# Kernel tuning notes

Measured on AMD Instinct MI355X. Metric: run time of the kernel, lower is better.

Reference implementation:

```python
import jax, jax.numpy as jnp
import numpy as np


def setup_inputs() -> dict:
    key = jax.random.key(0)
    B, T, FFT, HOP = 16, 2048, 1024, 256
    n_bins = FFT // 2 + 1  # 513
    stfts = jax.random.normal(key, (B, T, n_bins, 2), dtype=jnp.float32)
    return {"stfts": stfts, "frame_length": FFT, "frame_step": HOP, "fft_length": FFT}


def reference(stfts, frame_length, frame_step, fft_length):
    # --- precomputed constants (built in the layer's build()) ---
    n = jnp.arange(fft_length, dtype=jnp.float32)
    angles = (2.0 * np.pi / fft_length) * (n[:, None] * n[None, :])  # [fft, fft]
    idft_cos = jnp.cos(angles)
    idft_sin = jnp.sin(angles)
    # periodic Hann window
    t = jnp.arange(frame_length, dtype=jnp.float32)
    window = 0.5 - 0.5 * jnp.cos(2.0 * np.pi * t / frame_length)
    hop_ratio = frame_step / frame_length
    normalization = np.sqrt(1.0 / (1.0 - hop_ratio + 1e-8))
    syn_window = window / np.float32(normalization)
    if fft_length > frame_length:
        syn_window = jnp.pad(syn_window, (0, fft_length - frame_length))

    # --- forward ---
    real_part = stfts[..., 0]  # [B, T, n_bins]
    imag_part = stfts[..., 1]
    if fft_length % 2 == 0:
        mirror_real = real_part[:, :, 1:-1]
        mirror_imag = imag_part[:, :, 1:-1]
    else:
        mirror_real = real_part[:, :, 1:]
        mirror_imag = imag_part[:, :, 1:]
    full_real = jnp.concatenate([real_part, mirror_real[:, :, ::-1]], axis=-1)   # [B, T, fft]
    full_imag = jnp.concatenate([imag_part, -mirror_imag[:, :, ::-1]], axis=-1)  # [B, T, fft]

    # explicit IDFT via dense matmul (transpose_b in TF; matrices are symmetric)
    time_real = jnp.einsum('btf,nf->btn', full_real, idft_cos)
    time_real = time_real - jnp.einsum('btf,nf->btn', full_imag, idft_sin)
    time_real = time_real / jnp.float32(fft_length)

    windowed = (time_real * syn_window[None, None, :])[:, :, :frame_length]  # [B, T, frame_length]

    # overlap-and-add
    B, T, L = windowed.shape
    out_len = (T - 1) * frame_step + frame_length
    idx = jnp.arange(T)[:, None] * frame_step + jnp.arange(L)[None, :]  # [T, L]
    out = jnp.zeros((B, out_len), dtype=windowed.dtype).at[:, idx].add(windowed)
    return out
```

## Files before the change

### kernel.cpp

```cpp
#include <hip/hip_runtime.h>
#include <math.h>


#define BATCH  16
#define TFR    2048
#define NB     513
#define HOP    256
#define OUTLEN 525056
#define TROWS  2051
#define OWN    32
#define NBLK   65
#define OLALEN (OWN * HOP)
#define OLAPAD (OLALEN + OLALEN / 16)

#define NTHR   512
#define NWAVE  8

#define PIDX(n) ((n) + ((n) >> 4))

#define TWO_PI 6.2831853071795864f
#define WSCALE 8.456302966727588e-4f

__device__ __forceinline__ float2 cadd(float2 a, float2 b){ return make_float2(a.x+b.x, a.y+b.y); }
__device__ __forceinline__ float2 csub(float2 a, float2 b){ return make_float2(a.x-b.x, a.y-b.y); }
__device__ __forceinline__ float2 cmul(float2 a, float2 b){ return make_float2(a.x*b.x - a.y*b.y, a.x*b.y + a.y*b.x); }

#if __has_builtin(__builtin_amdgcn_permlane32_swap)
#define HAVE_PL32 1
__device__ __forceinline__ float plsel32(float v, bool pick0) {
    auto r = __builtin_amdgcn_permlane32_swap(
        __builtin_bit_cast(int, v), __builtin_bit_cast(int, v), false, false);
    return __builtin_bit_cast(float, pick0 ? r[0] : r[1]);
}
#else
#define HAVE_PL32 0
#endif

template<int CTRL>
__device__ __forceinline__ float dppf(float v) {
    return __builtin_bit_cast(float,
        __builtin_amdgcn_update_dpp(0, __builtin_bit_cast(int, v), CTRL, 0xF, 0xF, true));
}

__device__ __forceinline__ float2 bstep(float2 u, float2 p, bool hi, float2 W) {
    const float2 s = cadd(u, p);
    const float2 d = cmul(csub(u, p), W);
    return hi ? d : s;
}

__device__ __constant__ const float W16C[8] = { 1.f, 0.9238795325112867f, 0.7071067811865476f, 0.3826834323650898f,
                                                0.f,-0.3826834323650898f,-0.7071067811865476f,-0.9238795325112867f };
__device__ __constant__ const float W16S[8] = { 0.f, 0.3826834323650898f, 0.7071067811865476f, 0.9238795325112867f,
                                                1.f, 0.9238795325112867f, 0.7071067811865476f, 0.3826834323650898f };
__device__ __constant__ const float CWT[16] = {
    1.f, 0.9999811752826011f, 0.9999247018391445f, 0.9998305817958234f,
    0.9996988186962042f, 0.9995294175010931f, 0.9993223845883495f, 0.9990777277526454f,
    0.9987954562051724f, 0.9984755805732948f, 0.9981181129001492f, 0.9977230666441916f,
    0.9972904566786902f, 0.9968202992911657f, 0.9963126121827780f, 0.9957674144676598f };
__device__ __constant__ const float SWT[16] = {
    0.f, 0.0061358846491545f, 0.0122715382857199f, 0.0184067299058048f,
    0.0245412285229123f, 0.0306748031766366f, 0.0368072229413588f, 0.0429382569349408f,
    0.0490676743274180f, 0.0551952443496899f, 0.0613207363022086f, 0.0674439195636641f,
    0.0735645635996674f, 0.0796824379714301f, 0.0857973123444399f, 0.0919089564971327f };

__global__ __launch_bounds__(NTHR)
void istft_rfft(const float2* __restrict__ stfts, float* __restrict__ out)
{
    __shared__ float ola[OLAPAD];

    const int tid  = threadIdx.x;
    const int lane = tid & 63;
    const int wave = tid >> 6;

    const int b  = blockIdx.x / NBLK;
    const int ib = blockIdx.x - b * NBLK;
    const int T0 = ib * OWN;

    for (int i = tid; i < OLAPAD; i += NTHR) ola[i] = 0.f;

    float2 P, V;
    { float s, c; sincosf(TWO_PI * (float)lane * (1.0f/1024.0f), &s, &c); P = make_float2(c, s); }
    const int brl = ((lane & 1) << 5) | ((lane & 2) << 3) | ((lane & 4) << 1)
                  | ((lane & 8) >> 1) | ((lane & 16) >> 3) | ((lane & 32) >> 5);
    const int n0 = brl * 16;
    { float s, c; sincosf(TWO_PI * (float)n0 * (1.0f/1024.0f), &s, &c); V = make_float2(c, s); }

    const float2 Q   = cmul(P, P);
    const float2 P4  = cmul(Q, Q);
    const float2 P8  = cmul(P4, P4);
    const float2 B64 = cmul(P8, P8);
    const float2 B32 = cmul(B64, B64);
    const float2 B16 = cmul(B32, B32);
    const float2 B8c = cmul(B16, B16);
    const float2 B4c = cmul(B8c, B8c);

#if HAVE_PL32
    bool pick32;
    { auto pr = __builtin_amdgcn_permlane32_swap(lane, lane, false, false);
      pick32 = ((pr[0] == (lane & 31)) == (lane >= 32)); }
#endif
    const bool hi32 = lane >= 32;
    const bool hi16 = (lane & 16) != 0;
    const bool hi8  = (lane & 8)  != 0;
    const bool hi4  = (lane & 4)  != 0;
    const bool hi2  = (lane & 2)  != 0;
    const bool hi1  = (lane & 1)  != 0;

    __syncthreads();

    const int tmin = (T0 - 3 > 0) ? T0 - 3 : 0;
    const int tmax = (T0 + OWN - 1 < TFR - 1) ? T0 + OWN - 1 : TFR - 1;
    const int srcl = (64 - lane) & 63;

    for (int t = tmin + wave; t <= tmax; t += NWAVE) {
        const float2* Xg = stfts + (size_t)(b * TFR + t) * NB;

        float2 X[8];
        #pragma unroll
        for (int r = 0; r < 8; ++r) X[r] = Xg[lane + 64 * r];
        const float2 X512 = Xg[512];

        float2 Z[8];
        #pragma unroll
        for (int r = 0; r < 8; ++r) {
            float2 mv;
            mv.x = __shfl(X[7 - r].x, srcl);
            mv.y = __shfl(X[7 - r].y, srcl);
            const float2 fix = (r == 0) ? X512 : X[(8 - r) & 7];
            if (lane == 0) mv = fix;
            float Yy = X[r].y, Cy = -mv.y;
            if (lane == 0 && r == 0) { Yy = 0.f; Cy = 0.f; }
            const float Sx = X[r].x + mv.x, Sy = Yy + Cy;
            const float Dx = X[r].x - mv.x, Dy = Yy - Cy;
            const float2 W = cmul(P, make_float2(W16C[r], W16S[r]));
            const float ex = W.x * Dx - W.y * Dy;
            const float ey = W.x * Dy + W.y * Dx;
            Z[r] = make_float2(Sx - ey, Sy + ex);
        }

        float2 u[8];
        {
            const float2 t0 = cadd(Z[0], Z[4]), t1 = csub(Z[0], Z[4]);
            const float2 t2 = cadd(Z[2], Z[6]), t3 = csub(Z[2], Z[6]);
            const float2 t4 = cadd(Z[1], Z[5]), t5 = csub(Z[1], Z[5]);
            const float2 t6 = cadd(Z[3], Z[7]), t7 = csub(Z[3], Z[7]);
            const float2 E0 = cadd(t0, t2), E2 = csub(t0, t2);
            const float2 E1 = make_float2(t1.x - t3.y, t1.y + t3.x);
            const float2 E3 = make_float2(t1.x + t3.y, t1.y - t3.x);
            const float2 O0 = cadd(t4, t6), O2 = csub(t4, t6);
            const float2 O1 = make_float2(t5.x - t7.y, t5.y + t7.x);
            const float2 O3 = make_float2(t5.x + t7.y, t5.y - t7.x);
            const float cc = 0.70710678118654752f;
            const float2 W1O1 = make_float2(cc * (O1.x - O1.y), cc * (O1.x + O1.y));
            const float2 iO2  = make_float2(-O2.y, O2.x);
            const float2 W3O3 = make_float2(cc * (-O3.x - O3.y), cc * (O3.x - O3.y));
            u[0] = cadd(E0, O0);   u[4] = csub(E0, O0);
            u[1] = cadd(E1, W1O1); u[5] = csub(E1, W1O1);
            u[2] = cadd(E2, iO2);  u[6] = csub(E2, iO2);
            u[3] = cadd(E3, W3O3); u[7] = csub(E3, W3O3);
        }
        {
            const float2 om3 = cmul(P4, Q);
            const float2 om5 = cmul(P8, Q);
            const float2 om6 = cmul(P8, P4);
            const float2 om7 = cmul(P8, om3);
            u[1] = cmul(u[1], Q);
            u[2] = cmul(u[2], P4);
            u[3] = cmul(u[3], om3);
            u[4] = cmul(u[4], P8);
            u[5] = cmul(u[5], om5);
            u[6] = cmul(u[6], om6);
            u[7] = cmul(u[7], om7);
        }

        #pragma unroll
        for (int m = 0; m < 8; ++m) {
            float2 p;
#if HAVE_PL32
            p = make_float2(plsel32(u[m].x, pick32), plsel32(u[m].y, pick32));
#else
            p = make_float2(__shfl_xor(u[m].x, 32), __shfl_xor(u[m].y, 32));
#endif
            u[m] = bstep(u[m], p, hi32, B64);
        }
        #pragma unroll
        for (int m = 0; m < 8; ++m) {
            const float2 p = make_float2(__shfl_xor(u[m].x, 16), __shfl_xor(u[m].y, 16));
            u[m] = bstep(u[m], p, hi16, B32);
        }
        #pragma unroll
        for (int m = 0; m < 8; ++m) {
            const float2 p = make_float2(dppf<0x128>(u[m].x), dppf<0x128>(u[m].y));
            u[m] = bstep(u[m], p, hi8, B16);
        }
        #pragma unroll
        for (int m = 0; m < 8; ++m) {
            const float2 p = make_float2(__shfl_xor(u[m].x, 4), __shfl_xor(u[m].y, 4));
            u[m] = bstep(u[m], p, hi4, B8c);
        }
        #pragma unroll
        for (int m = 0; m < 8; ++m) {
            const float2 p = make_float2(dppf<0x4E>(u[m].x), dppf<0x4E>(u[m].y));
            u[m] = bstep(u[m], p, hi2, B4c);
        }
        #pragma unroll
        for (int m = 0; m < 8; ++m) {
            const float2 p = make_float2(dppf<0xB1>(u[m].x), dppf<0xB1>(u[m].y));
            u[m] = hi1 ? csub(p, u[m]) : cadd(u[m], p);
        }

        const int base = (t - T0) * HOP + n0;
        if ((unsigned)base < OLALEN) {
            const int pb = PIDX(base);
            #pragma unroll
            for (int m = 0; m < 8; ++m) {
                const float w0 = 0.5f * WSCALE * (1.f - (V.x * CWT[2*m]   - V.y * SWT[2*m]));
                const float w1 = 0.5f * WSCALE * (1.f - (V.x * CWT[2*m+1] - V.y * SWT[2*m+1]));
                atomicAdd(&ola[pb + 2*m],     u[m].x * w0);
                atomicAdd(&ola[pb + 2*m + 1], u[m].y * w1);
            }
        }
    }

    __syncthreads();

    const int ownRows = (TROWS - T0 < OWN) ? (TROWS - T0) : OWN;
    const int total   = ownRows * HOP;
    float* og = out + (size_t)b * OUTLEN + (size_t)T0 * HOP;
    for (int i = tid; i < total; i += NTHR)
        og[i] = ola[PIDX(i)];
}

extern "C" void kernel_launch(void* const* d_in, const int* in_sizes, int n_in,
                              void* d_out, int out_size, void* d_ws, size_t ws_size,
                              hipStream_t stream)
{
    const float2* stfts = reinterpret_cast<const float2*>(d_in[0]);
    float* out = reinterpret_cast<float*>(d_out);

    istft_rfft<<<dim3(BATCH * NBLK), dim3(NTHR), 0, stream>>>(stfts, out);
}
```

Before: 206.0 us.

## Load two frames per iteration, read mirrored bins directly, use cheaper lane permutes

Each wave now loads two STFT frames up front before running the FFT on either, so more global-load latency can overlap with compute. The mirrored conjugate half is read straight from global memory at reversed indices rather than built with cross-lane shuffles. The xor-16 and xor-4 butterfly exchanges switch from __shfl_xor to permlane16_swap and ds_swizzle. This raises register pressure because two frames are held at once, and it doubles the number of global loads per frame, though the mirrored reads should mostly hit cache.

```diff
diff --git a/kernel.cpp b/kernel.cpp
--- a/kernel.cpp
+++ b/kernel.cpp
@@ -36,10 +36,25 @@
 #define HAVE_PL32 0
 #endif
 
+#if __has_builtin(__builtin_amdgcn_permlane16_swap)
+#define HAVE_PL16 1
+__device__ __forceinline__ float plsel16(float v, bool pick0) {
+    auto r = __builtin_amdgcn_permlane16_swap(
+        __builtin_bit_cast(int, v), __builtin_bit_cast(int, v), false, false);
+    return __builtin_bit_cast(float, pick0 ? r[0] : r[1]);
+}
+#else
+#define HAVE_PL16 0
+#endif
+
 template<int CTRL>
 __device__ __forceinline__ float dppf(float v) {
     return __builtin_bit_cast(float,
         __builtin_amdgcn_update_dpp(0, __builtin_bit_cast(int, v), CTRL, 0xF, 0xF, true));
+}
+__device__ __forceinline__ float swz4(float v) {
+    return __builtin_bit_cast(float,
+        __builtin_amdgcn_ds_swizzle(__builtin_bit_cast(int, v), 0x101F));
 }
 
 __device__ __forceinline__ float2 bstep(float2 u, float2 p, bool hi, float2 W) {
@@ -97,7 +112,12 @@
 #if HAVE_PL32
     bool pick32;
     { auto pr = __builtin_amdgcn_permlane32_swap(lane, lane, false, false);
-      pick32 = ((pr[0] == (lane & 31)) == (lane >= 32)); }
+      pick32 = (pr[0] == (lane ^ 32)); }
+#endif
+#if HAVE_PL16
+    bool pick16;
+    { auto pr = __builtin_amdgcn_permlane16_swap(lane, lane, false, false);
+      pick16 = (pr[0] == (lane ^ 16)); }
 #endif
     const bool hi32 = lane >= 32;
     const bool hi16 = (lane & 16) != 0;
@@ -110,24 +130,12 @@
 
     const int tmin = (T0 - 3 > 0) ? T0 - 3 : 0;
     const int tmax = (T0 + OWN - 1 < TFR - 1) ? T0 + OWN - 1 : TFR - 1;
-    const int srcl = (64 - lane) & 63;
-
-    for (int t = tmin + wave; t <= tmax; t += NWAVE) {
-        const float2* Xg = stfts + (size_t)(b * TFR + t) * NB;
-
-        float2 X[8];
-        #pragma unroll
-        for (int r = 0; r < 8; ++r) X[r] = Xg[lane + 64 * r];
-        const float2 X512 = Xg[512];
-
+
+    auto frameProc = [&](const float2* X, const float2* XM, int t) {
         float2 Z[8];
         #pragma unroll
         for (int r = 0; r < 8; ++r) {
-            float2 mv;
-            mv.x = __shfl(X[7 - r].x, srcl);
-            mv.y = __shfl(X[7 - r].y, srcl);
-            const float2 fix = (r == 0) ? X512 : X[(8 - r) & 7];
-            if (lane == 0) mv = fix;
+            const float2 mv = XM[r];
             float Yy = X[r].y, Cy = -mv.y;
             if (lane == 0 && r == 0) { Yy = 0.f; Cy = 0.f; }
             const float Sx = X[r].x + mv.x, Sy = Yy + Cy;
@@ -185,7 +193,12 @@
         }
         #pragma unroll
         for (int m = 0; m < 8; ++m) {
-            const float2 p = make_float2(__shfl_xor(u[m].x, 16), __shfl_xor(u[m].y, 16));
+            float2 p;
+#if HAVE_PL16
+            p = make_float2(plsel16(u[m].x, pick16), plsel16(u[m].y, pick16));
+#else
+            p = make_float2(__shfl_xor(u[m].x, 16), __shfl_xor(u[m].y, 16));
+#endif
             u[m] = bstep(u[m], p, hi16, B32);
         }
         #pragma unroll
@@ -195,7 +208,7 @@
         }
         #pragma unroll
         for (int m = 0; m < 8; ++m) {
-            const float2 p = make_float2(__shfl_xor(u[m].x, 4), __shfl_xor(u[m].y, 4));
+            const float2 p = make_float2(swz4(u[m].x), swz4(u[m].y));
             u[m] = bstep(u[m], p, hi4, B8c);
         }
         #pragma unroll
@@ -220,6 +233,29 @@
                 atomicAdd(&ola[pb + 2*m + 1], u[m].y * w1);
             }
         }
+    };
+
+    for (int t = tmin + wave; t <= tmax; t += 2 * NWAVE) {
+        const int  tb = t + NWAVE;
+        const bool vb = (tb <= tmax);
+
+        const float2* Ga = stfts + (size_t)(b * TFR + t) * NB;
+        const float2* Gb = stfts + (size_t)(b * TFR + (vb ? tb : t)) * NB;
+
+        float2 Xa[8], Ma[8], Xb[8], Mb[8];
+        #pragma unroll
+        for (int r = 0; r < 8; ++r) {
+            Xa[r] = Ga[lane + 64 * r];
+            Ma[r] = Ga[512 - 64 * r - lane];
+        }
+        #pragma unroll
+        for (int r = 0; r < 8; ++r) {
+            Xb[r] = Gb[lane + 64 * r];
+            Mb[r] = Gb[512 - 64 * r - lane];
+        }
+
+        frameProc(Xa, Ma, t);
+        if (vb) frameProc(Xb, Mb, tb);
     }
 
     __syncthreads();
```

New measurement: 203.9 us. About the same (-1.0%).
